# Performance work log

Hardware: AMD Instinct MI355X
Metric: run time of the kernel (lower is better)

## Reference

```python
import jax, jax.numpy as jnp
import numpy as np

V, E, Hdim, T, B = 32000, 1024, 1024, 64, 32

def setup_inputs() -> dict:
    key = jax.random.key(0)
    ks = jax.random.split(key, 8)
    return {
        "input_x": jax.random.randint(ks[0], (B, T), 0, V, dtype=jnp.int64),
        "initial_state": jnp.zeros((B, Hdim), dtype=jnp.float32),
        "emb": jax.random.normal(ks[1], (V, E), dtype=jnp.float32) * 0.02,
        "H": jax.random.normal(ks[2], (Hdim, Hdim), dtype=jnp.float32) * 0.02,
        "I": jax.random.normal(ks[3], (E, Hdim), dtype=jnp.float32) * 0.02,
        "b1": jax.random.normal(ks[4], (1, Hdim), dtype=jnp.float32) * 0.02,
        "U": jax.random.normal(ks[5], (Hdim, V), dtype=jnp.float32) * 0.02,
        "b2": jax.random.normal(ks[6], (1, V), dtype=jnp.float32) * 0.02,
    }

def reference(input_x, initial_state, emb, H, I, b1, U, b2):
    # Embedding lookup: [B,T] -> [T,B,E] (scan over time)
    x = emb[input_x]                      # [B,T,E]
    x = jnp.transpose(x, (1, 0, 2))       # [T,B,E]

    def step(h, x_t):
        h = jax.nn.sigmoid(h @ H + x_t @ I + b1)  # Elman cell
        return h, h

    final_state, hs = jax.lax.scan(step, initial_state, x)  # hs: [T,B,Hdim]
    # Projection to vocab logits (dropout is identity at eval / p=0)
    logits = jnp.einsum('tbh,hv->tbv', hs, U) + b2          # [T,B,V]
    return logits, final_state
```

## Files before the change

kernel.cpp:

```cpp
#include <hip/hip_runtime.h>


typedef _Float16 f16;
typedef f16 f16x4 __attribute__((ext_vector_type(4)));
typedef f16 f16x8 __attribute__((ext_vector_type(8)));
typedef float f32x4 __attribute__((ext_vector_type(4)));

static constexpr int Vv = 32000, Ee = 1024, Hd = 1024, Tt = 64, Bb = 32;
static constexpr int Mm = Tt * Bb;

#define GLOAD16(g, l)                                                          \
  __builtin_amdgcn_global_load_lds(                                            \
      (const __attribute__((address_space(1))) void*)(g),                      \
      (__attribute__((address_space(3))) void*)(l), 16, 0, 0)


__global__ void transpose_cvt(const float* __restrict__ in, f16* __restrict__ out,
                              int K, int N) {
  __shared__ float t[32][33];
  int n0 = blockIdx.x * 32, k0 = blockIdx.y * 32;
  int tx = threadIdx.x, ty = threadIdx.y;
#pragma unroll
  for (int i = 0; i < 32; i += 8)
    t[ty + i][tx] = in[(size_t)(k0 + ty + i) * N + n0 + tx];
  __syncthreads();
#pragma unroll
  for (int i = 0; i < 32; i += 8)
    out[(size_t)(n0 + ty + i) * K + k0 + tx] = (f16)t[tx][ty + i];
}

__global__ void gather_emb(const int* __restrict__ tok, const float* __restrict__ emb,
                           f16* __restrict__ xg) {
  int m = blockIdx.x;
  int b = m % Bb, t = m / Bb;
  int token = tok[b * Tt + t];
  const float* src = emb + (size_t)token * Ee;
  f16* dst = xg + (size_t)m * Ee;
  int e = threadIdx.x * 4;
  float4 v = *(const float4*)(src + e);
  f16x4 o = {(f16)v.x, (f16)v.y, (f16)v.z, (f16)v.w};
  *(f16x4*)(dst + e) = o;
}

__global__ void cvt_h0(const float* __restrict__ h0, f16* __restrict__ h0f) {
  int i = blockIdx.x * 256 + threadIdx.x;
  h0f[i] = (f16)h0[i];
}

__global__ __launch_bounds__(256) void gemm_f16(
    const f16* __restrict__ A, const f16* __restrict__ Bt,
    const float* __restrict__ bias, float* __restrict__ C, int M, int N, int K) {
  __shared__ __align__(16) f16 As[128 * 64];
  __shared__ __align__(16) f16 Bs[128 * 64];

  const int nwg = gridDim.x, bid = blockIdx.x;
  const int cpx = nwg >> 3;
  const int i = (bid & 7) * cpx + (bid >> 3);
  const int ntm = M >> 7;
  const int tm = i % ntm, tn = i / ntm;

  const int tid = threadIdx.x;
  const int lane = tid & 63, wid = tid >> 6;
  const int wm = wid >> 1, wn = wid & 1;

  const int srow = lane >> 3;
  const int sslot = (lane & 7) ^ srow;
  const f16* gA = A + (size_t)(tm * 128 + wid * 8 + srow) * K + sslot * 8;
  const f16* gB = Bt + (size_t)(tn * 128 + wid * 8 + srow) * K + sslot * 8;
  f16* lA = As + wid * 8 * 64;
  f16* lB = Bs + wid * 8 * 64;

  f32x4 acc[4][4] = {};
  const int r = lane & 15, kb = lane >> 4;

  for (int kc = 0; kc < K; kc += 64) {
    __syncthreads();
#pragma unroll
    for (int rr = 0; rr < 4; ++rr) {
      GLOAD16(gA + (size_t)rr * 32 * K + kc, lA + rr * 2048);
      GLOAD16(gB + (size_t)rr * 32 * K + kc, lB + rr * 2048);
    }
    __syncthreads();

#pragma unroll
    for (int kk = 0; kk < 2; ++kk) {
      f16x8 af[4], bf[4];
#pragma unroll
      for (int ii = 0; ii < 4; ++ii) {
        const int rowA = wm * 64 + ii * 16 + r;
        const int rowB = wn * 64 + ii * 16 + r;
        const int slot = ((kk * 4 + kb) ^ (r & 7)) * 8;
        af[ii] = *(const f16x8*)(As + rowA * 64 + slot);
        bf[ii] = *(const f16x8*)(Bs + rowB * 64 + slot);
      }
#pragma unroll
      for (int ii = 0; ii < 4; ++ii)
#pragma unroll
        for (int jj = 0; jj < 4; ++jj)
          acc[ii][jj] = __builtin_amdgcn_mfma_f32_16x16x32_f16(af[ii], bf[jj], acc[ii][jj], 0, 0, 0);
    }
  }

  const int col0 = tn * 128 + wn * 64, row0 = tm * 128 + wm * 64;
#pragma unroll
  for (int ii = 0; ii < 4; ++ii)
#pragma unroll
    for (int jj = 0; jj < 4; ++jj) {
      int c = col0 + jj * 16 + (lane & 15);
      int rbase = row0 + ii * 16 + (lane >> 4) * 4;
      float bv = bias ? bias[c] : 0.f;
#pragma unroll
      for (int rr = 0; rr < 4; ++rr)
        C[(size_t)(rbase + rr) * N + c] = acc[ii][jj][rr] + bv;
    }
}

#define BAR __builtin_amdgcn_s_barrier()
#define LG0 asm volatile("s_waitcnt lgkmcnt(0)")

__global__ __launch_bounds__(512) void gemm256(
    const f16* __restrict__ A, const f16* __restrict__ Bt,
    const float* __restrict__ bias, float* __restrict__ C,
    int M, int N, int K) {
  __shared__ __align__(16) f16 sm[65536];

  const int nwg = gridDim.x, bid = blockIdx.x;
  const int cpx = nwg >> 3;
  const int ii = (bid & 7) * cpx + (bid >> 3);
  const int ntm = M >> 8;
  const int tm = ii % ntm, tn = ii / ntm;

  const int tid = threadIdx.x;
  const int lane = tid & 63, w = tid >> 6;
  const int wm = w >> 2, wn = w & 3;
  const int r = lane & 15, kb = lane >> 4;

  const int srow = tid >> 3;
  const int slot8 = ((tid & 7) ^ (srow & 7)) * 8;
  const f16* gA = A + (size_t)(tm * 256 + srow) * K + slot8;
  const f16* gB = Bt + (size_t)(tn * 256 + srow) * K + slot8;
  const int lw = w * 512;

  const int NK = K >> 6;

  f32x4 acc[8][4] = {};
  f16x8 a[4][2], b[4][2];

#define STG(kt, ab, R0)                                                        \
  do {                                                                         \
    const f16* gsrc = (ab) ? gB : gA;                                          \
    f16* lb = sm + ((kt) & 1) * 32768 + (ab) * 16384 + (R0) * 64 + lw;         \
    GLOAD16(gsrc + (size_t)(R0) * K + (kt) * 64, lb);                          \
    GLOAD16(gsrc + (size_t)((R0) + 64) * K + (kt) * 64, lb + 4096);            \
  } while (0)

#define LDA(MH)                                                                \
  _Pragma("unroll") for (int i = 0; i < 4; ++i)                                \
  _Pragma("unroll") for (int kk = 0; kk < 2; ++kk)                             \
      a[i][kk] = *(const f16x8*)(Abuf + (wm * 128 + (MH) * 64 + i * 16 + r) * 64 + \
                                 (((kk * 4 + kb) ^ (r & 7)) * 8));

#define LDB(J0)                                                                \
  _Pragma("unroll") for (int j = 0; j < 2; ++j)                                \
  _Pragma("unroll") for (int kk = 0; kk < 2; ++kk)                             \
      b[(J0) + j][kk] = *(const f16x8*)(Bbuf + (wn * 64 + ((J0) + j) * 16 + r) * 64 + \
                                        (((kk * 4 + kb) ^ (r & 7)) * 8));

#define MFMA_Q(MI0, J0)                                                        \
  __builtin_amdgcn_s_setprio(1);                                               \
  _Pragma("unroll") for (int mi = 0; mi < 4; ++mi)                             \
  _Pragma("unroll") for (int j = 0; j < 2; ++j)                                \
  _Pragma("unroll") for (int kk = 0; kk < 2; ++kk)                             \
      acc[(MI0) + mi][(J0) + j] = __builtin_amdgcn_mfma_f32_16x16x32_f16(      \
          a[mi][kk], b[(J0) + j][kk], acc[(MI0) + mi][(J0) + j], 0, 0, 0);     \
  __builtin_amdgcn_s_setprio(0);

  STG(0, 0, 0); STG(0, 0, 128);
  STG(0, 1, 0); STG(0, 1, 128);
  STG(1, 0, 0); STG(1, 0, 128);
  asm volatile("s_waitcnt vmcnt(4)");
  BAR;

  for (int k = 0; k < NK; ++k) {
    const f16* Abuf = sm + (k & 1) * 32768;
    const f16* Bbuf = Abuf + 16384;
    const int kn1 = (k + 1 == NK) ? 0 : k + 1;
    const int kn2 = (k + 2 >= NK) ? k + 2 - NK : k + 2;

    LDA(0); LDB(0);
    STG(kn1, 1, 0);
    BAR; LG0;
    MFMA_Q(0, 0);
    BAR;

    LDB(2);
    STG(kn1, 1, 128);
    BAR; LG0;
    MFMA_Q(0, 2);
    BAR;

    LDA(1);
    BAR; LG0;
    MFMA_Q(4, 2);
    BAR;

    STG(kn2, 0, 0); STG(kn2, 0, 128);
    BAR;
    MFMA_Q(4, 0);
    asm volatile("s_waitcnt vmcnt(4)");
    BAR;
  }

#pragma unroll
  for (int mi = 0; mi < 8; ++mi)
#pragma unroll
    for (int j = 0; j < 4; ++j) {
      int c = tn * 256 + wn * 64 + j * 16 + r;
      int rbase = tm * 256 + wm * 128 + mi * 16 + kb * 4;
      float bv = bias[c];
#pragma unroll
      for (int q = 0; q < 4; ++q)
        C[(size_t)(rbase + q) * N + c] = acc[mi][j][q] + bv;
    }
#undef STG
#undef LDA
#undef LDB
#undef MFMA_Q
}

__global__ __launch_bounds__(256) void recurrence_mfma(
    const f16* __restrict__ Ht,
    const float* __restrict__ xI,
    const f16* __restrict__ h0f,
    f16* __restrict__ hs,
    float* __restrict__ hN,
    int* __restrict__ cnt) {
  __shared__ float red[4][512];
  const int tid = threadIdx.x;
  const int lane = tid & 63, w = tid >> 6;
  const int bn = blockIdx.x;
  const int nb = gridDim.x;
  const int r = lane & 15, kb = lane >> 4;
  const int colg = bn * 16 + r;

  f16x8 bH[8];
#pragma unroll
  for (int ks = 0; ks < 8; ++ks)
    bH[ks] = *(const f16x8*)(Ht + (size_t)colg * Hd + w * 256 + ks * 32 + kb * 8);

  const int eb = tid >> 3, ecp = tid & 7;

  for (int t = 0; t < Tt; ++t) {
    const f16* hp = t ? hs + (size_t)(t - 1) * Bb * Hd : h0f;
    const float2 xv = *(const float2*)(xI + (size_t)(t * Bb + eb) * Hd + bn * 16 + 2 * ecp);
    f32x4 acc[2] = {};
#pragma unroll
    for (int mt = 0; mt < 2; ++mt) {
      f16x8 af[8];
#pragma unroll
      for (int ks = 0; ks < 8; ++ks)
        af[ks] = *(const f16x8*)(hp + (size_t)(mt * 16 + r) * Hd + w * 256 + ks * 32 + kb * 8);
#pragma unroll
      for (int ks = 0; ks < 8; ++ks)
        acc[mt] = __builtin_amdgcn_mfma_f32_16x16x32_f16(af[ks], bH[ks], acc[mt], 0, 0, 0);
    }
#pragma unroll
    for (int mt = 0; mt < 2; ++mt)
#pragma unroll
      for (int q = 0; q < 4; ++q)
        red[w][mt * 256 + (kb * 4 + q) * 16 + r] = acc[mt][q];
    __syncthreads();

    {
      const float2 r0 = *(const float2*)&red[0][eb * 16 + 2 * ecp];
      const float2 r1 = *(const float2*)&red[1][eb * 16 + 2 * ecp];
      const float2 r2 = *(const float2*)&red[2][eb * 16 + 2 * ecp];
      const float2 r3 = *(const float2*)&red[3][eb * 16 + 2 * ecp];
      float v0 = r0.x + r1.x + r2.x + r3.x + xv.x;
      float v1 = r0.y + r1.y + r2.y + r3.y + xv.y;
      float s0 = 1.f / (1.f + __expf(-v0));
      float s1 = 1.f / (1.f + __expf(-v1));
      union { f16 h[2]; unsigned u; } pk;
      pk.h[0] = (f16)s0;
      pk.h[1] = (f16)s1;
      unsigned* dst = (unsigned*)(hs + (size_t)(t * Bb + eb) * Hd + bn * 16 + 2 * ecp);
      __hip_atomic_store(dst, pk.u, __ATOMIC_RELAXED, __HIP_MEMORY_SCOPE_AGENT);
      if (t == Tt - 1)
        *(float2*)(hN + (size_t)eb * Hd + bn * 16 + 2 * ecp) = make_float2(s0, s1);
    }

    __syncthreads();
    if (tid == 0)
      (void)__hip_atomic_fetch_add(cnt, 1, __ATOMIC_RELAXED, __HIP_MEMORY_SCOPE_AGENT);
    const int target = (t + 1) * nb;
    while (__hip_atomic_load(cnt, __ATOMIC_RELAXED, __HIP_MEMORY_SCOPE_AGENT) < target)
      __builtin_amdgcn_s_sleep(1);
  }
}

extern "C" void kernel_launch(void* const* d_in, const int* in_sizes, int n_in,
                              void* d_out, int out_size, void* d_ws, size_t ws_size,
                              hipStream_t stream) {
  const int* input_x = (const int*)d_in[0];
  const float* h0 = (const float*)d_in[1];
  const float* emb = (const float*)d_in[2];
  const float* Hm = (const float*)d_in[3];
  const float* Im = (const float*)d_in[4];
  const float* b1 = (const float*)d_in[5];
  const float* Um = (const float*)d_in[6];
  const float* b2 = (const float*)d_in[7];
  float* out = (float*)d_out;

  char* ws = (char*)d_ws;
  size_t off = 0;
  auto alloc = [&](size_t bytes) { void* p = ws + off; off = (off + bytes + 255) & ~(size_t)255; return p; };
  f16* Ut = (f16*)alloc((size_t)Vv * Hd * 2);
  f16* It = (f16*)alloc((size_t)Hd * Ee * 2);
  f16* Ht = (f16*)alloc((size_t)Hd * Hd * 2);
  f16* xg = (f16*)alloc((size_t)Mm * Ee * 2);
  float* xI = (float*)alloc((size_t)Mm * Hd * 4);
  f16* hs = (f16*)alloc((size_t)Mm * Hd * 2);
  f16* h0f = (f16*)alloc((size_t)Bb * Hd * 2);
  int* cnt = (int*)alloc(256);
  (void)ws_size; (void)in_sizes; (void)n_in; (void)out_size;

  hipMemsetAsync(cnt, 0, sizeof(int), stream);

  transpose_cvt<<<dim3(Vv / 32, Hd / 32), dim3(32, 8), 0, stream>>>(Um, Ut, Hd, Vv);
  transpose_cvt<<<dim3(Hd / 32, Ee / 32), dim3(32, 8), 0, stream>>>(Im, It, Ee, Hd);
  transpose_cvt<<<dim3(Hd / 32, Hd / 32), dim3(32, 8), 0, stream>>>(Hm, Ht, Hd, Hd);
  gather_emb<<<Mm, 256, 0, stream>>>(input_x, emb, xg);
  cvt_h0<<<(Bb * Hd) / 256, 256, 0, stream>>>(h0, h0f);

  gemm_f16<<<(Mm / 128) * (Hd / 128), 256, 0, stream>>>(xg, It, b1, xI, Mm, Hd, Ee);

  recurrence_mfma<<<64, 256, 0, stream>>>(Ht, xI, h0f, hs, out + (size_t)Mm * Vv, cnt);

  gemm256<<<(Mm / 256) * (Vv / 256), 512, 0, stream>>>(hs, Ut, b2, out, Mm, Vv, Hd);
}
```

Baseline: 494.4 us.

## Overlap U transpose-convert with recurrence via extra blocks in one launch

The large U transpose/convert to f16 is moved into the recurrence kernel, running on 192 extra blocks while 64 blocks perform the latency-bound serial recurrence, so the two overlap instead of running back to back. The spin barrier now counts only the recurrence blocks, and a compiler memory fence is added after the wait. The logits GEMM also switches its output stores to nontemporal stores to avoid polluting cache. The risk is that the transpose blocks compete with the recurrence for memory bandwidth and slow its critical path, and it relies on all recurrence blocks being co-resident.

After: 467.2 us. 5.5% less time.

```diff
diff --git a/kernel.cpp b/kernel.cpp
--- a/kernel.cpp
+++ b/kernel.cpp
@@ -8,6 +8,8 @@
 
 static constexpr int Vv = 32000, Ee = 1024, Hd = 1024, Tt = 64, Bb = 32;
 static constexpr int Mm = Tt * Bb;
+static constexpr int NBR = 64;
+static constexpr int NBT = 192;
 
 #define GLOAD16(g, l)                                                          \
   __builtin_amdgcn_global_load_lds(                                            \
@@ -220,7 +222,8 @@
       float bv = bias[c];
 #pragma unroll
       for (int q = 0; q < 4; ++q)
-        C[(size_t)(rbase + q) * N + c] = acc[mi][j][q] + bv;
+        __builtin_nontemporal_store(acc[mi][j][q] + bv,
+                                    C + (size_t)(rbase + q) * N + c);
     }
 #undef STG
 #undef LDA
@@ -228,18 +231,40 @@
 #undef MFMA_Q
 }
 
-__global__ __launch_bounds__(256) void recurrence_mfma(
+__global__ __launch_bounds__(256) void rec_plus_transpose(
     const f16* __restrict__ Ht,
     const float* __restrict__ xI,
     const f16* __restrict__ h0f,
     f16* __restrict__ hs,
     float* __restrict__ hN,
-    int* __restrict__ cnt) {
+    int* __restrict__ cnt,
+    const float* __restrict__ Um,
+    f16* __restrict__ Ut) {
   __shared__ float red[4][512];
+  __shared__ float tt[32][33];
   const int tid = threadIdx.x;
+
+  if (blockIdx.x >= NBR) {
+    const int tb = blockIdx.x - NBR;
+    const int tx = tid & 31, ty = tid >> 5;
+    const int ntile_n = Vv / 32;
+    const int ntiles = ntile_n * (Hd / 32);
+    for (int tile = tb; tile < ntiles; tile += NBT) {
+      const int n0 = (tile % ntile_n) * 32, k0 = (tile / ntile_n) * 32;
+#pragma unroll
+      for (int i = 0; i < 32; i += 8)
+        tt[ty + i][tx] = Um[(size_t)(k0 + ty + i) * Vv + n0 + tx];
+      __syncthreads();
+#pragma unroll
+      for (int i = 0; i < 32; i += 8)
+        Ut[(size_t)(n0 + ty + i) * Hd + k0 + tx] = (f16)tt[tx][ty + i];
+      __syncthreads();
+    }
+    return;
+  }
+
   const int lane = tid & 63, w = tid >> 6;
   const int bn = blockIdx.x;
-  const int nb = gridDim.x;
   const int r = lane & 15, kb = lane >> 4;
   const int colg = bn * 16 + r;
 
@@ -292,9 +317,10 @@
     __syncthreads();
     if (tid == 0)
       (void)__hip_atomic_fetch_add(cnt, 1, __ATOMIC_RELAXED, __HIP_MEMORY_SCOPE_AGENT);
-    const int target = (t + 1) * nb;
+    const int target = (t + 1) * NBR;
     while (__hip_atomic_load(cnt, __ATOMIC_RELAXED, __HIP_MEMORY_SCOPE_AGENT) < target)
       __builtin_amdgcn_s_sleep(1);
+    asm volatile("" ::: "memory");
   }
 }
 
@@ -326,7 +352,6 @@
 
   hipMemsetAsync(cnt, 0, sizeof(int), stream);
 
-  transpose_cvt<<<dim3(Vv / 32, Hd / 32), dim3(32, 8), 0, stream>>>(Um, Ut, Hd, Vv);
   transpose_cvt<<<dim3(Hd / 32, Ee / 32), dim3(32, 8), 0, stream>>>(Im, It, Ee, Hd);
   transpose_cvt<<<dim3(Hd / 32, Hd / 32), dim3(32, 8), 0, stream>>>(Hm, Ht, Hd, Hd);
   gather_emb<<<Mm, 256, 0, stream>>>(input_x, emb, xg);
@@ -334,7 +359,8 @@
 
   gemm_f16<<<(Mm / 128) * (Hd / 128), 256, 0, stream>>>(xg, It, b1, xI, Mm, Hd, Ee);
 
-  recurrence_mfma<<<64, 256, 0, stream>>>(Ht, xI, h0f, hs, out + (size_t)Mm * Vv, cnt);
+  rec_plus_transpose<<<NBR + NBT, 256, 0, stream>>>(
+      Ht, xI, h0f, hs, out + (size_t)Mm * Vv, cnt, Um, Ut);
 
   gemm256<<<(Mm / 256) * (Vv / 256), 512, 0, stream>>>(hs, Ut, b2, out, Mm, Vv, Hd);
 }
```
